# Kernel tuning notes

Hardware: AMD Instinct MI355X
Metric: run time of the kernel (lower is better)

## Reference

```python
import jax, jax.numpy as jnp
import numpy as np


def _lstm_scan(x, w_ih, w_hh, b_ih, b_hh):
    """Unidirectional LSTM, PyTorch gate order (i, f, g, o).
    x: [B, T, C]; w_ih: [4H, C]; w_hh: [4H, H]. Returns [B, T, H]."""
    H = w_hh.shape[1]
    # Precompute input contribution for all timesteps (one big GEMM).
    xg = jnp.einsum('btc,gc->btg', x, w_ih) + b_ih + b_hh  # [B, T, 4H]

    def step(carry, xg_t):
        h, c = carry
        gates = xg_t + h @ w_hh.T
        i, f, g, o = jnp.split(gates, 4, axis=-1)
        c = jax.nn.sigmoid(f) * c + jax.nn.sigmoid(i) * jnp.tanh(g)
        h = jax.nn.sigmoid(o) * jnp.tanh(c)
        return (h, c), h

    B = x.shape[0]
    h0 = jnp.zeros((B, H), x.dtype)
    _, hs = jax.lax.scan(step, (h0, h0), jnp.swapaxes(xg, 0, 1))
    return jnp.swapaxes(hs, 0, 1)  # [B, T, H]


def _bilstm(x, w_ih_f, w_hh_f, b_ih_f, b_hh_f, w_ih_b, w_hh_b, b_ih_b, b_hh_b):
    fwd = _lstm_scan(x, w_ih_f, w_hh_f, b_ih_f, b_hh_f)
    bwd = _lstm_scan(x[:, ::-1], w_ih_b, w_hh_b, b_ih_b, b_hh_b)[:, ::-1]
    return jnp.concatenate([fwd, bwd], axis=-1)  # [B, T, 2H]


def setup_inputs() -> dict:
    key = jax.random.key(0)
    B, Hh, Ww, C, Hd = 64, 48, 48, 192, 48
    ks = jax.random.split(key, 20)
    s = 1.0 / np.sqrt(Hd)  # PyTorch LSTM init scale
    inp = {"x": jax.random.normal(ks[0], (B, Hh, Ww, C), jnp.float32)}
    names = ["v_w_ih_f", "v_w_hh_f", "v_b_ih_f", "v_b_hh_f",
             "v_w_ih_b", "v_w_hh_b", "v_b_ih_b", "v_b_hh_b",
             "h_w_ih_f", "h_w_hh_f", "h_b_ih_f", "h_b_hh_f",
             "h_w_ih_b", "h_w_hh_b", "h_b_ih_b", "h_b_hh_b"]
    shapes = [(4 * Hd, C), (4 * Hd, Hd), (4 * Hd,), (4 * Hd,)] * 4
    for i, (n, sh) in enumerate(zip(names, shapes)):
        inp[n] = jax.random.uniform(ks[1 + i], sh, jnp.float32, -s, s)
    inp["proj_w"] = jax.random.uniform(ks[17], (C, 4 * Hd), jnp.float32, -s, s)
    inp["proj_b"] = jax.random.uniform(ks[18], (C,), jnp.float32, -s, s)
    return inp


def reference(x, v_w_ih_f, v_w_hh_f, v_b_ih_f, v_b_hh_f,
              v_w_ih_b, v_w_hh_b, v_b_ih_b, v_b_hh_b,
              h_w_ih_f, h_w_hh_f, h_b_ih_f, h_b_hh_f,
              h_w_ih_b, h_w_hh_b, h_b_ih_b, h_b_hh_b,
              proj_w, proj_b):
    B, Hh, Ww, C = x.shape
    # Vertical: scan over height for each column.
    xv = jnp.transpose(x, (0, 2, 1, 3)).reshape(B * Ww, Hh, C)
    v = _bilstm(xv, v_w_ih_f, v_w_hh_f, v_b_ih_f, v_b_hh_f,
                v_w_ih_b, v_w_hh_b, v_b_ih_b, v_b_hh_b)
    v = jnp.transpose(v.reshape(B, Ww, Hh, -1), (0, 2, 1, 3))  # [B,H,W,2Hd]
    # Horizontal: scan over width for each row.
    xh = x.reshape(B * Hh, Ww, C)
    h = _bilstm(xh, h_w_ih_f, h_w_hh_f, h_b_ih_f, h_b_hh_f,
                h_w_ih_b, h_w_hh_b, h_b_ih_b, h_b_hh_b)
    h = h.reshape(B, Hh, Ww, -1)  # [B,H,W,2Hd]
    combined = jnp.concatenate([v, h], axis=-1)  # [B,H,W,4Hd]
    return jnp.einsum('bhwk,ck->bhwc', combined, proj_w) + proj_b
```

## Files before the change

kernel.cpp:

```cpp
#include <hip/hip_runtime.h>

typedef short short8 __attribute__((ext_vector_type(8)));
typedef float f32x4 __attribute__((ext_vector_type(4)));
typedef unsigned short u16;

__device__ __forceinline__ u16 f2bf(float f) {
  unsigned int u = __builtin_bit_cast(unsigned int, f);
  u = (u + 0x7FFFu + ((u >> 16) & 1u)) >> 16;
  return (u16)u;
}

__device__ __forceinline__ short8 cvt8(float4 a, float4 b) {
  short8 v;
  v[0] = (short)f2bf(a.x); v[1] = (short)f2bf(a.y);
  v[2] = (short)f2bf(a.z); v[3] = (short)f2bf(a.w);
  v[4] = (short)f2bf(b.x); v[5] = (short)f2bf(b.y);
  v[6] = (short)f2bf(b.z); v[7] = (short)f2bf(b.w);
  return v;
}

__device__ __forceinline__ float sigmoidf_fast(float x) {
  return __builtin_amdgcn_rcpf(1.0f + __expf(-x));
}
__device__ __forceinline__ float tanhf_fast(float x) {
  return 1.0f - 2.0f * __builtin_amdgcn_rcpf(1.0f + __expf(2.0f * x));
}

__global__ __launch_bounds__(192, 1)
void bilstm_scan_kernel(
    const float* __restrict__ x,
    const float* __restrict__ wih_vf, const float* __restrict__ whh_vf,
    const float* __restrict__ bih_vf, const float* __restrict__ bhh_vf,
    const float* __restrict__ wih_vb, const float* __restrict__ whh_vb,
    const float* __restrict__ bih_vb, const float* __restrict__ bhh_vb,
    const float* __restrict__ wih_hf, const float* __restrict__ whh_hf,
    const float* __restrict__ bih_hf, const float* __restrict__ bhh_hf,
    const float* __restrict__ wih_hb, const float* __restrict__ whh_hb,
    const float* __restrict__ bih_hb, const float* __restrict__ bhh_hb,
    u16* __restrict__ comb)
{
  __shared__ u16 lds[61440];
  u16* Alds = lds;
  u16* Blds = lds + 12288;

  const int tid  = threadIdx.x;
  const int lane = tid & 63;
  const int wv   = tid >> 6;
  const int cl   = lane & 15;
  const int kg   = lane >> 4;
  const int dir  = blockIdx.x >> 6;
  const int blk  = blockIdx.x & 63;
  const int base = blk * 48;
  const bool vert = dir < 2;
  const bool bwd  = (dir & 1) != 0;

  const float *wih, *whh, *bih, *bhh;
  if      (dir == 0) { wih = wih_vf; whh = whh_vf; bih = bih_vf; bhh = bhh_vf; }
  else if (dir == 1) { wih = wih_vb; whh = whh_vb; bih = bih_vb; bhh = bhh_vb; }
  else if (dir == 2) { wih = wih_hf; whh = whh_hf; bih = bih_hf; bhh = bhh_hf; }
  else               { wih = wih_hb; whh = whh_hb; bih = bih_hb; bhh = bhh_hb; }

  for (int i = 0; i < 32; ++i) {
    int ch = tid + 192 * i;
    int n  = ch >> 5;
    int k0 = (ch & 31) << 3;
    short8 v = {};
    if (k0 < 192) {
      const float4* s0 = (const float4*)(wih + n * 192 + k0);
      v = cvt8(s0[0], s0[1]);
    } else if (k0 < 240) {
      const float4* s0 = (const float4*)(whh + n * 48 + (k0 - 192));
      v = cvt8(s0[0], s0[1]);
    }
    *(short8*)(&Blds[(n * 256 + k0) ^ ((n & 7) << 3)]) = v;
  }
  for (int i = 0; i < 2; ++i) {
    int ch = tid + 192 * i;
    int s  = ch >> 3;
    int k0 = 192 + ((ch & 7) << 3);
    short8 z = {};
    *(short8*)(&Alds[(s * 256 + k0) ^ ((s & 7) << 3)]) = z;
  }
  float bias[4];
  #pragma unroll
  for (int g = 0; g < 4; ++g) {
    int col = g * 48 + wv * 16 + cl;
    bias[g] = bih[col] + bhh[col];
  }

  auto stage_x = [&](int tt) {
    int tp = bwd ? 47 - tt : tt;
    #pragma unroll
    for (int i = 0; i < 6; ++i) {
      int ch = tid + 192 * i;
      int s  = ch / 24;
      int k0 = (ch % 24) << 3;
      int sq = base + s;
      int bb = sq / 48;
      int rc = sq - bb * 48;
      size_t poff = vert ? (size_t)((bb * 48 + tp) * 48 + rc) * 192
                         : (size_t)((bb * 48 + rc) * 48 + tp) * 192;
      const float4* sp = (const float4*)(x + poff + k0);
      float4 u0 = sp[0], u1 = sp[1];
      *(short8*)(&Alds[(s * 256 + k0) ^ ((s & 7) << 3)]) = cvt8(u0, u1);
    }
  };
  stage_x(0);

  float c[12];
  #pragma unroll
  for (int i = 0; i < 12; ++i) c[i] = 0.0f;

  const int hd = wv * 16 + cl;

  for (int t = 0; t < 48; ++t) {
    __syncthreads();

    f32x4 acc[3][4] = {};
    #pragma unroll
    for (int kk = 0; kk < 8; ++kk) {
      int krow = kk * 32 + kg * 8;
      short8 af[3], bf[4];
      #pragma unroll
      for (int mi = 0; mi < 3; ++mi) {
        int row = mi * 16 + cl;
        af[mi] = *(const short8*)(&Alds[(row * 256 + krow) ^ ((row & 7) << 3)]);
      }
      #pragma unroll
      for (int g = 0; g < 4; ++g) {
        int col = g * 48 + wv * 16 + cl;
        bf[g] = *(const short8*)(&Blds[(col * 256 + krow) ^ ((col & 7) << 3)]);
      }
      #pragma unroll
      for (int mi = 0; mi < 3; ++mi)
        #pragma unroll
        for (int g = 0; g < 4; ++g)
          acc[mi][g] = __builtin_amdgcn_mfma_f32_16x16x32_bf16(
              af[mi], bf[g], acc[mi][g], 0, 0, 0);
    }
    __syncthreads();

    int tp = bwd ? 47 - t : t;
    if (t < 47) stage_x(t + 1);

    #pragma unroll
    for (int mi = 0; mi < 3; ++mi) {
      #pragma unroll
      for (int r = 0; r < 4; ++r) {
        int s = mi * 16 + kg * 4 + r;
        float xi = acc[mi][0][r] + bias[0];
        float xf = acc[mi][1][r] + bias[1];
        float xg = acc[mi][2][r] + bias[2];
        float xo = acc[mi][3][r] + bias[3];
        float ii = sigmoidf_fast(xi);
        float ff = sigmoidf_fast(xf);
        float gg = tanhf_fast(xg);
        float oo = sigmoidf_fast(xo);
        float cc = ff * c[mi * 4 + r] + ii * gg;
        c[mi * 4 + r] = cc;
        float hh = oo * tanhf_fast(cc);
        u16 hb = f2bf(hh);
        Alds[(s * 256 + 192 + hd) ^ ((s & 7) << 3)] = hb;
        int sq = base + s;
        int bb = sq / 48;
        int rc = sq - bb * 48;
        int p = vert ? (bb * 48 + tp) * 48 + rc : (bb * 48 + rc) * 48 + tp;
        comb[(size_t)p * 192 + dir * 48 + hd] = hb;
      }
    }
  }
}

__global__ __launch_bounds__(256, 1)
void proj_kernel(const u16* __restrict__ comb,
                 const float* __restrict__ pw,
                 const float* __restrict__ pb,
                 float* __restrict__ out)
{
  __shared__ u16 lds[49152];
  u16* Alds = lds;
  u16* Blds = lds + 12288;

  const int tid = threadIdx.x;
  const int lane = tid & 63;
  const int wv = tid >> 6;
  const int cl = lane & 15;
  const int kg = lane >> 4;
  const size_t p0 = (size_t)blockIdx.x * 64;

  for (int i = 0; i < 18; ++i) {
    int ch = tid + 256 * i;
    int n  = ch / 24;
    int k0 = (ch % 24) << 3;
    const float4* s0 = (const float4*)(pw + n * 192 + k0);
    *(short8*)(&Blds[(n * 192 + k0) ^ ((n & 7) << 3)]) = cvt8(s0[0], s0[1]);
  }
  for (int i = 0; i < 6; ++i) {
    int ch = tid + 256 * i;
    int s  = ch / 24;
    int k0 = (ch % 24) << 3;
    short8 v = *(const short8*)(comb + (p0 + s) * 192 + k0);
    *(short8*)(&Alds[(s * 192 + k0) ^ ((s & 7) << 3)]) = v;
  }
  float pbr[3];
  #pragma unroll
  for (int ni = 0; ni < 3; ++ni) pbr[ni] = pb[wv * 48 + ni * 16 + cl];

  __syncthreads();

  f32x4 acc[4][3] = {};
  #pragma unroll
  for (int kk = 0; kk < 6; ++kk) {
    int krow = kk * 32 + kg * 8;
    short8 af[4], bf[3];
    #pragma unroll
    for (int mi = 0; mi < 4; ++mi) {
      int row = mi * 16 + cl;
      af[mi] = *(const short8*)(&Alds[(row * 192 + krow) ^ ((row & 7) << 3)]);
    }
    #pragma unroll
    for (int ni = 0; ni < 3; ++ni) {
      int col = wv * 48 + ni * 16 + cl;
      bf[ni] = *(const short8*)(&Blds[(col * 192 + krow) ^ ((col & 7) << 3)]);
    }
    #pragma unroll
    for (int mi = 0; mi < 4; ++mi)
      #pragma unroll
      for (int ni = 0; ni < 3; ++ni)
        acc[mi][ni] = __builtin_amdgcn_mfma_f32_16x16x32_bf16(
            af[mi], bf[ni], acc[mi][ni], 0, 0, 0);
  }

  #pragma unroll
  for (int mi = 0; mi < 4; ++mi)
    #pragma unroll
    for (int ni = 0; ni < 3; ++ni)
      #pragma unroll
      for (int r = 0; r < 4; ++r) {
        size_t o = (p0 + mi * 16 + kg * 4 + r) * 192 + wv * 48 + ni * 16 + cl;
        out[o] = acc[mi][ni][r] + pbr[ni];
      }
}

extern "C" void kernel_launch(void* const* d_in, const int* in_sizes, int n_in,
                              void* d_out, int out_size, void* d_ws, size_t ws_size,
                              hipStream_t stream) {
  const float* x = (const float*)d_in[0];
  u16* comb = (u16*)d_ws;

  bilstm_scan_kernel<<<256, 192, 0, stream>>>(
      x,
      (const float*)d_in[1],  (const float*)d_in[2],  (const float*)d_in[3],  (const float*)d_in[4],
      (const float*)d_in[5],  (const float*)d_in[6],  (const float*)d_in[7],  (const float*)d_in[8],
      (const float*)d_in[9],  (const float*)d_in[10], (const float*)d_in[11], (const float*)d_in[12],
      (const float*)d_in[13], (const float*)d_in[14], (const float*)d_in[15], (const float*)d_in[16],
      comb);

  proj_kernel<<<2304, 256, 0, stream>>>(
      comb, (const float*)d_in[17], (const float*)d_in[18], (float*)d_out);
}
```

Before: 229.5 us.

## Hoist input-gate GEMM out of LSTM scan into a separate parallel kernel

Splits the fused scan into a dedicated xg GEMM kernel that computes input contributions for all four directions at once and stores them as bf16, followed by a scan kernel where each wave handles 16 sequences and multiplies only by the small recurrent weights held in registers. This takes the 192-wide input projection off the serial critical path and replaces block-level barriers with per-wave LDS exchange. The cost is a large bf16 intermediate written to and read from global memory, and an extra rounding of the gate preactivations.

```diff
diff --git a/kernel.cpp b/kernel.cpp
--- a/kernel.cpp
+++ b/kernel.cpp
@@ -1,6 +1,7 @@
 #include <hip/hip_runtime.h>
 
 typedef short short8 __attribute__((ext_vector_type(8)));
+typedef short short4v __attribute__((ext_vector_type(4)));
 typedef float f32x4 __attribute__((ext_vector_type(4)));
 typedef unsigned short u16;
 
@@ -9,7 +10,10 @@
   u = (u + 0x7FFFu + ((u >> 16) & 1u)) >> 16;
   return (u16)u;
 }
-
+__device__ __forceinline__ float bf2f(u16 h) {
+  unsigned int u = ((unsigned int)h) << 16;
+  return __builtin_bit_cast(float, u);
+}
 __device__ __forceinline__ short8 cvt8(float4 a, float4 b) {
   short8 v;
   v[0] = (short)f2bf(a.x); v[1] = (short)f2bf(a.y);
@@ -18,7 +22,12 @@
   v[6] = (short)f2bf(b.z); v[7] = (short)f2bf(b.w);
   return v;
 }
-
+__device__ __forceinline__ short4v pack4(f32x4 a) {
+  short4v v;
+  v[0] = (short)f2bf(a[0]); v[1] = (short)f2bf(a[1]);
+  v[2] = (short)f2bf(a[2]); v[3] = (short)f2bf(a[3]);
+  return v;
+}
 __device__ __forceinline__ float sigmoidf_fast(float x) {
   return __builtin_amdgcn_rcpf(1.0f + __expf(-x));
 }
@@ -26,148 +35,201 @@
   return 1.0f - 2.0f * __builtin_amdgcn_rcpf(1.0f + __expf(2.0f * x));
 }
 
-__global__ __launch_bounds__(192, 1)
-void bilstm_scan_kernel(
-    const float* __restrict__ x,
-    const float* __restrict__ wih_vf, const float* __restrict__ whh_vf,
-    const float* __restrict__ bih_vf, const float* __restrict__ bhh_vf,
-    const float* __restrict__ wih_vb, const float* __restrict__ whh_vb,
-    const float* __restrict__ bih_vb, const float* __restrict__ bhh_vb,
-    const float* __restrict__ wih_hf, const float* __restrict__ whh_hf,
-    const float* __restrict__ bih_hf, const float* __restrict__ bhh_hf,
-    const float* __restrict__ wih_hb, const float* __restrict__ whh_hb,
-    const float* __restrict__ bih_hb, const float* __restrict__ bhh_hb,
-    u16* __restrict__ comb)
+__global__ __launch_bounds__(512, 1)
+void xg_gemm_kernel(const float* __restrict__ x,
+    const float* __restrict__ w0, const float* __restrict__ w1,
+    const float* __restrict__ w2, const float* __restrict__ w3,
+    const float* __restrict__ bi0, const float* __restrict__ bh0,
+    const float* __restrict__ bi1, const float* __restrict__ bh1,
+    const float* __restrict__ bi2, const float* __restrict__ bh2,
+    const float* __restrict__ bi3, const float* __restrict__ bh3,
+    u16* __restrict__ xg)
 {
-  __shared__ u16 lds[61440];
-  u16* Alds = lds;
-  u16* Blds = lds + 12288;
-
+  __shared__ u16 xl[2][3072];
   const int tid  = threadIdx.x;
   const int lane = tid & 63;
   const int wv   = tid >> 6;
   const int cl   = lane & 15;
   const int kg   = lane >> 4;
-  const int dir  = blockIdx.x >> 6;
-  const int blk  = blockIdx.x & 63;
-  const int base = blk * 48;
+  const int dir  = wv >> 1;
+  const int nbase = (wv & 1) * 96;
+
+  const float* wp  = dir == 0 ? w0 : dir == 1 ? w1 : dir == 2 ? w2 : w3;
+  const float* bip = dir == 0 ? bi0 : dir == 1 ? bi1 : dir == 2 ? bi2 : bi3;
+  const float* bhp = dir == 0 ? bh0 : dir == 1 ? bh1 : dir == 2 ? bh2 : bh3;
+
+  short8 wf[6][6];
+  #pragma unroll
+  for (int nt = 0; nt < 6; ++nt) {
+    int n = nbase + nt * 16 + cl;
+    #pragma unroll
+    for (int kk = 0; kk < 6; ++kk) {
+      const float4* p = (const float4*)(wp + n * 192 + kk * 32 + kg * 8);
+      wf[nt][kk] = cvt8(p[0], p[1]);
+    }
+  }
+  f32x4 bv[6];
+  #pragma unroll
+  for (int nt = 0; nt < 6; ++nt)
+    #pragma unroll
+    for (int r = 0; r < 4; ++r) {
+      int n = nbase + nt * 16 + kg * 4 + r;
+      bv[nt][r] = bip[n] + bhp[n];
+    }
+
+  const int spx = tid / 24;
+  const int sk  = (tid % 24) * 8;
+  float4 sa, sb;
+
+  auto sload = [&](int it) {
+    if (tid < 384) {
+      const float4* p = (const float4*)(x + (size_t)((blockIdx.x * 36 + it) * 16 + spx) * 192 + sk);
+      sa = p[0]; sb = p[1];
+    }
+  };
+  auto swrite = [&](int b) {
+    if (tid < 384) {
+      int idx = (spx * 192 + sk) ^ ((spx & 7) << 3);
+      *(short8*)&xl[b][idx] = cvt8(sa, sb);
+    }
+  };
+
+  sload(0); swrite(0); __syncthreads();
+
+  int buf = 0;
+  for (int it = 0; it < 36; ++it) {
+    if (it < 35) sload(it + 1);
+    const int pxb = (blockIdx.x * 36 + it) * 16;
+
+    f32x4 acc[6];
+    #pragma unroll
+    for (int nt = 0; nt < 6; ++nt) acc[nt] = bv[nt];
+    #pragma unroll
+    for (int kk = 0; kk < 6; ++kk) {
+      int idx = (cl * 192 + kk * 32 + kg * 8) ^ ((cl & 7) << 3);
+      short8 bfr = *(const short8*)&xl[buf][idx];
+      #pragma unroll
+      for (int nt = 0; nt < 6; ++nt)
+        acc[nt] = __builtin_amdgcn_mfma_f32_16x16x32_bf16(wf[nt][kk], bfr, acc[nt], 0, 0, 0);
+    }
+    #pragma unroll
+    for (int nt = 0; nt < 6; ++nt) {
+      size_t o = (size_t)(pxb + cl) * 768 + dir * 192 + nbase + nt * 16 + kg * 4;
+      *(short4v*)(xg + o) = pack4(acc[nt]);
+    }
+    __syncthreads();
+    if (it < 35) swrite(buf ^ 1);
+    __syncthreads();
+    buf ^= 1;
+  }
+}
+
+__global__ __launch_bounds__(256, 1)
+void scan_kernel(const u16* __restrict__ xg,
+    const float* __restrict__ u0, const float* __restrict__ u1,
+    const float* __restrict__ u2, const float* __restrict__ u3,
+    u16* __restrict__ comb)
+{
+  __shared__ u16 hl[4][16 * 72];
+  const int tid  = threadIdx.x;
+  const int lane = tid & 63;
+  const int wv   = tid >> 6;
+  const int cl   = lane & 15;
+  const int kg   = lane >> 4;
+  const int W    = blockIdx.x * 4 + wv;
+  const int dir  = W / 192;
+  const int g    = W - dir * 192;
+  const int bb   = g / 3;
+  const int rc   = (g - bb * 3) * 16 + cl;
   const bool vert = dir < 2;
   const bool bwd  = (dir & 1) != 0;
 
-  const float *wih, *whh, *bih, *bhh;
-  if      (dir == 0) { wih = wih_vf; whh = whh_vf; bih = bih_vf; bhh = bhh_vf; }
-  else if (dir == 1) { wih = wih_vb; whh = whh_vb; bih = bih_vb; bhh = bhh_vb; }
-  else if (dir == 2) { wih = wih_hf; whh = whh_hf; bih = bih_hf; bhh = bhh_hf; }
-  else               { wih = wih_hb; whh = whh_hb; bih = bih_hb; bhh = bhh_hb; }
-
-  for (int i = 0; i < 32; ++i) {
-    int ch = tid + 192 * i;
-    int n  = ch >> 5;
-    int k0 = (ch & 31) << 3;
-    short8 v = {};
-    if (k0 < 192) {
-      const float4* s0 = (const float4*)(wih + n * 192 + k0);
-      v = cvt8(s0[0], s0[1]);
-    } else if (k0 < 240) {
-      const float4* s0 = (const float4*)(whh + n * 48 + (k0 - 192));
-      v = cvt8(s0[0], s0[1]);
-    }
-    *(short8*)(&Blds[(n * 256 + k0) ^ ((n & 7) << 3)]) = v;
-  }
-  for (int i = 0; i < 2; ++i) {
-    int ch = tid + 192 * i;
-    int s  = ch >> 3;
-    int k0 = 192 + ((ch & 7) << 3);
-    short8 z = {};
-    *(short8*)(&Alds[(s * 256 + k0) ^ ((s & 7) << 3)]) = z;
-  }
-  float bias[4];
-  #pragma unroll
-  for (int g = 0; g < 4; ++g) {
-    int col = g * 48 + wv * 16 + cl;
-    bias[g] = bih[col] + bhh[col];
-  }
-
-  auto stage_x = [&](int tt) {
-    int tp = bwd ? 47 - tt : tt;
-    #pragma unroll
-    for (int i = 0; i < 6; ++i) {
-      int ch = tid + 192 * i;
-      int s  = ch / 24;
-      int k0 = (ch % 24) << 3;
-      int sq = base + s;
-      int bb = sq / 48;
-      int rc = sq - bb * 48;
-      size_t poff = vert ? (size_t)((bb * 48 + tp) * 48 + rc) * 192
-                         : (size_t)((bb * 48 + rc) * 48 + tp) * 192;
-      const float4* sp = (const float4*)(x + poff + k0);
-      float4 u0 = sp[0], u1 = sp[1];
-      *(short8*)(&Alds[(s * 256 + k0) ^ ((s & 7) << 3)]) = cvt8(u0, u1);
-    }
-  };
-  stage_x(0);
+  const float* up = dir == 0 ? u0 : dir == 1 ? u1 : dir == 2 ? u2 : u3;
+
+  short8 uf[12][2];
+  #pragma unroll
+  for (int nt = 0; nt < 12; ++nt) {
+    int n = nt * 16 + cl;
+    {
+      const float4* p = (const float4*)(up + n * 48 + kg * 8);
+      uf[nt][0] = cvt8(p[0], p[1]);
+    }
+    if (kg < 2) {
+      const float4* p = (const float4*)(up + n * 48 + 32 + kg * 8);
+      uf[nt][1] = cvt8(p[0], p[1]);
+    } else {
+      short8 z = {}; uf[nt][1] = z;
+    }
+  }
+
+  u16* hrow = &hl[wv][0];
+  for (int i = 0; i < 18; ++i) hrow[lane * 18 + i] = 0;
 
   float c[12];
   #pragma unroll
-  for (int i = 0; i < 12; ++i) c[i] = 0.0f;
-
-  const int hd = wv * 16 + cl;
+  for (int i = 0; i < 12; ++i) c[i] = 0.f;
+
+  const int tp0 = bwd ? 47 : 0;
+  int px = vert ? (bb * 48 + tp0) * 48 + rc : (bb * 48 + rc) * 48 + tp0;
+  const int dpx = (vert ? 48 : 1) * (bwd ? -1 : 1);
+
+  short4v xb[12];
+  {
+    const u16* xp = xg + (size_t)px * 768 + dir * 192 + kg * 4;
+    #pragma unroll
+    for (int nt = 0; nt < 12; ++nt)
+      xb[nt] = *(const short4v*)(xp + nt * 16);
+  }
 
   for (int t = 0; t < 48; ++t) {
-    __syncthreads();
-
-    f32x4 acc[3][4] = {};
-    #pragma unroll
-    for (int kk = 0; kk < 8; ++kk) {
-      int krow = kk * 32 + kg * 8;
-      short8 af[3], bf[4];
-      #pragma unroll
-      for (int mi = 0; mi < 3; ++mi) {
-        int row = mi * 16 + cl;
-        af[mi] = *(const short8*)(&Alds[(row * 256 + krow) ^ ((row & 7) << 3)]);
-      }
-      #pragma unroll
-      for (int g = 0; g < 4; ++g) {
-        int col = g * 48 + wv * 16 + cl;
-        bf[g] = *(const short8*)(&Blds[(col * 256 + krow) ^ ((col & 7) << 3)]);
-      }
-      #pragma unroll
-      for (int mi = 0; mi < 3; ++mi)
-        #pragma unroll
-        for (int g = 0; g < 4; ++g)
-          acc[mi][g] = __builtin_amdgcn_mfma_f32_16x16x32_bf16(
-              af[mi], bf[g], acc[mi][g], 0, 0, 0);
-    }
-    __syncthreads();
-
-    int tp = bwd ? 47 - t : t;
-    if (t < 47) stage_x(t + 1);
-
-    #pragma unroll
-    for (int mi = 0; mi < 3; ++mi) {
+    short8 hb0 = *(const short8*)&hl[wv][cl * 72 + kg * 8];
+    short8 hb1 = *(const short8*)&hl[wv][cl * 72 + 32 + kg * 8];
+
+    f32x4 acc[12];
+    #pragma unroll
+    for (int nt = 0; nt < 12; ++nt) {
+      f32x4 a;
+      a[0] = bf2f((u16)xb[nt][0]); a[1] = bf2f((u16)xb[nt][1]);
+      a[2] = bf2f((u16)xb[nt][2]); a[3] = bf2f((u16)xb[nt][3]);
+      acc[nt] = a;
+    }
+    #pragma unroll
+    for (int nt = 0; nt < 12; ++nt)
+      acc[nt] = __builtin_amdgcn_mfma_f32_16x16x32_bf16(uf[nt][0], hb0, acc[nt], 0, 0, 0);
+    #pragma unroll
+    for (int nt = 0; nt < 12; ++nt)
+      acc[nt] = __builtin_amdgcn_mfma_f32_16x16x32_bf16(uf[nt][1], hb1, acc[nt], 0, 0, 0);
+
+    int pxn = px + dpx;
+    if (t < 47) {
+      const u16* xp = xg + (size_t)pxn * 768 + dir * 192 + kg * 4;
+      #pragma unroll
+      for (int nt = 0; nt < 12; ++nt)
+        xb[nt] = *(const short4v*)(xp + nt * 16);
+    }
+
+    #pragma unroll
+    for (int q = 0; q < 3; ++q) {
+      short4v h4;
       #pragma unroll
       for (int r = 0; r < 4; ++r) {
-        int s = mi * 16 + kg * 4 + r;
-        float xi = acc[mi][0][r] + bias[0];
-        float xf = acc[mi][1][r] + bias[1];
-        float xg = acc[mi][2][r] + bias[2];
-        float xo = acc[mi][3][r] + bias[3];
+        float xi  = acc[q][r];
+        float xf  = acc[3 + q][r];
+        float xgv = acc[6 + q][r];
+        float xo  = acc[9 + q][r];
         float ii = sigmoidf_fast(xi);
         float ff = sigmoidf_fast(xf);
-        float gg = tanhf_fast(xg);
+        float gg = tanhf_fast(xgv);
         float oo = sigmoidf_fast(xo);
-        float cc = ff * c[mi * 4 + r] + ii * gg;
-        c[mi * 4 + r] = cc;
+        float cc = ff * c[q * 4 + r] + ii * gg;
+        c[q * 4 + r] = cc;
         float hh = oo * tanhf_fast(cc);
-        u16 hb = f2bf(hh);
-        Alds[(s * 256 + 192 + hd) ^ ((s & 7) << 3)] = hb;
-        int sq = base + s;
-        int bb = sq / 48;
-        int rc = sq - bb * 48;
-        int p = vert ? (bb * 48 + tp) * 48 + rc : (bb * 48 + rc) * 48 + tp;
-        comb[(size_t)p * 192 + dir * 48 + hd] = hb;
+        h4[r] = (short)f2bf(hh);
       }
-    }
+      *(short4v*)&hl[wv][cl * 72 + q * 16 + kg * 4] = h4;
+      *(short4v*)&comb[(size_t)px * 192 + dir * 48 + q * 16 + kg * 4] = h4;
+    }
+    px = pxn;
   }
 }
 
@@ -246,14 +308,23 @@
                               void* d_out, int out_size, void* d_ws, size_t ws_size,
                               hipStream_t stream) {
   const float* x = (const float*)d_in[0];
-  u16* comb = (u16*)d_ws;
-
-  bilstm_scan_kernel<<<256, 192, 0, stream>>>(
+  u16* xg   = (u16*)d_ws;
+  u16* comb = (u16*)d_ws + (size_t)147456 * 768;
+
+  xg_gemm_kernel<<<256, 512, 0, stream>>>(
       x,
-      (const float*)d_in[1],  (const float*)d_in[2],  (const float*)d_in[3],  (const float*)d_in[4],
-      (const float*)d_in[5],  (const float*)d_in[6],  (const float*)d_in[7],  (const float*)d_in[8],
-      (const float*)d_in[9],  (const float*)d_in[10], (const float*)d_in[11], (const float*)d_in[12],
-      (const float*)d_in[13], (const float*)d_in[14], (const float*)d_in[15], (const float*)d_in[16],
+      (const float*)d_in[1], (const float*)d_in[5],
+      (const float*)d_in[9], (const float*)d_in[13],
+      (const float*)d_in[3],  (const float*)d_in[4],
+      (const float*)d_in[7],  (const float*)d_in[8],
+      (const float*)d_in[11], (const float*)d_in[12],
+      (const float*)d_in[15], (const float*)d_in[16],
+      xg);
+
+  scan_kernel<<<192, 256, 0, stream>>>(
+      xg,
+      (const float*)d_in[2], (const float*)d_in[6],
+      (const float*)d_in[10], (const float*)d_in[14],
       comb);
 
   proj_kernel<<<2304, 256, 0, stream>>>(
```

Result: slower. 321.9 us (+40.3%).
